# Performance work log

Hardware: AMD Instinct MI355X
Metric: run time of the kernel (lower is better)

## Reference

```python
import jax, jax.numpy as jnp
import numpy as np

N, E, D, ED, L, B = 100000, 1600000, 128, 16, 5, 64
EPS = 1e-5


def _layer_norm(x, w, b):
    mu = jnp.mean(x, axis=-1, keepdims=True)
    var = jnp.mean((x - mu) ** 2, axis=-1, keepdims=True)
    return (x - mu) * jax.lax.rsqrt(var + EPS) * w + b


def setup_inputs() -> dict:
    key = jax.random.key(0)
    ks = jax.random.split(key, 10)
    sc = 0.05
    s = jax.random.normal(ks[0], (N, D), jnp.float32)
    edge_index = jax.random.randint(ks[1], (2, E), 0, N, dtype=jnp.int64)
    edge_attr = jax.random.normal(ks[2], (E, ED), jnp.float32)
    batch = jnp.sort(jax.random.randint(ks[3], (N,), 0, B, dtype=jnp.int64))
    return dict(
        s=s, edge_index=edge_index, edge_attr=edge_attr, batch=batch,
        ln_w=jnp.ones((L, D), jnp.float32),
        ln_b=jnp.zeros((L, D), jnp.float32),
        eW1=jax.random.normal(ks[4], (L, 2 * D + ED, ED), jnp.float32) * sc,
        eb1=jnp.zeros((L, ED), jnp.float32),
        eW2=jax.random.normal(ks[5], (L, ED, ED), jnp.float32) * sc,
        eb2=jnp.zeros((L, ED), jnp.float32),
        nW1=jax.random.normal(ks[6], (L, D + ED, D), jnp.float32) * sc,
        nb1=jnp.zeros((L, D), jnp.float32),
        nW2=jax.random.normal(ks[7], (L, D, D), jnp.float32) * sc,
        nb2=jnp.zeros((L, D), jnp.float32),
    )


def reference(s, edge_index, edge_attr, batch, ln_w, ln_b, eW1, eb1, eW2, eb2, nW1, nb1, nW2, nb2):
    src, dst = edge_index[0], edge_index[1]
    n = s.shape[0]
    num_layers = ln_w.shape[0]
    # scatter-mean denominator (in-degree, clamped to 1)
    deg = jax.ops.segment_sum(jnp.ones((edge_index.shape[1],), s.dtype), dst, num_segments=n)
    deg = jnp.maximum(deg, 1.0)[:, None]
    for i in range(num_layers):
        # per-node LayerNorm over feature dim (vector channel is None)
        s = _layer_norm(s, ln_w[i], ln_b[i])
        # edge message: gather endpoints, concat with edge_attr -> [E, 2D+ED]
        m = jnp.concatenate([s[src], s[dst], edge_attr], axis=-1)
        edge_attr = jax.nn.silu(m @ eW1[i] + eb1[i]) @ eW2[i] + eb2[i]
        # scatter-mean aggregate to destination nodes -> [N, ED]
        agg = jax.ops.segment_sum(edge_attr, dst, num_segments=n) / deg
        h = jnp.concatenate([s, agg], axis=-1)
        out = jax.nn.silu(h @ nW1[i] + nb1[i]) @ nW2[i] + nb2[i]  # discarded, as in original
    return s, edge_attr
```

## Files before the change

kernel.cpp:

```cpp
#include <hip/hip_runtime.h>

#define N_NODES 100000
#define N_EDGES 1600000
#define DIM     128
#define EDIM    16
#define NLAYERS 5

typedef unsigned short ushort_t;
typedef short bf16x8 __attribute__((ext_vector_type(8)));
typedef float f32x4  __attribute__((ext_vector_type(4)));

__device__ __forceinline__ ushort_t f2bf(float f) {
    union { float f; unsigned int i; } c; c.f = f;
    unsigned int r = c.i + 0x7fffu + ((c.i >> 16) & 1u);
    return (ushort_t)(r >> 16);
}
__device__ __forceinline__ float lo_bf(unsigned int w) {
    union { unsigned int i; float f; } c; c.i = w << 16; return c.f;
}
__device__ __forceinline__ float hi_bf(unsigned int w) {
    union { unsigned int i; float f; } c; c.i = w & 0xffff0000u; return c.f;
}
__device__ __forceinline__ unsigned int pk_bf16(float lo, float hi) {
    unsigned int r;
    asm("v_cvt_pk_bf16_f32 %0, %1, %2" : "=v"(r) : "v"(lo), "v"(hi));
    return r;
}
__device__ __forceinline__ bf16x8 pk8(f32x4 a, f32x4 b) {
    union { unsigned int w[4]; bf16x8 v; } c;
    c.w[0] = pk_bf16(a[0], a[1]); c.w[1] = pk_bf16(a[2], a[3]);
    c.w[2] = pk_bf16(b[0], b[1]); c.w[3] = pk_bf16(b[2], b[3]);
    return c.v;
}
__device__ __forceinline__ void lds_fence() {
    asm volatile("s_waitcnt lgkmcnt(0)" ::: "memory");
    __builtin_amdgcn_sched_barrier(0);
}

__global__ void swizzle_weights(const float* __restrict__ eW1,
                                const float* __restrict__ eW2,
                                ushort_t* __restrict__ w1s,
                                ushort_t* __restrict__ w2s) {
    int id = blockIdx.x * 256 + threadIdx.x;
    if (id >= NLAYERS * 10 * 64) return;
    int lane = id & 63;
    int t10 = id >> 6;
    int layer = t10 / 10, t = t10 % 10;
    int n = lane & 15, quad = lane >> 4;
    if (t < 9) {
        ushort_t* dst = w1s + ((size_t)(layer * 9 + t) * 64 + lane) * 8;
        #pragma unroll
        for (int j = 0; j < 8; ++j) {
            int k = t * 32 + quad * 8 + j;
            dst[j] = (k < 2 * DIM + EDIM)
                       ? f2bf(eW1[((size_t)layer * 272 + k) * 16 + n])
                       : (ushort_t)0;
        }
    } else {
        ushort_t* dst = w2s + ((size_t)layer * 64 + lane) * 8;
        #pragma unroll
        for (int j = 0; j < 8; ++j) {
            int k = quad * 8 + j;
            dst[j] = (k < EDIM) ? f2bf(eW2[((size_t)layer * 16 + k) * 16 + n])
                                : (ushort_t)0;
        }
    }
}

__global__ __launch_bounds__(256) void ln_uv(
        const float* __restrict__ sin, float* __restrict__ sout,
        const float* __restrict__ lnw, const float* __restrict__ lnb,
        const ushort_t* __restrict__ w1s,
        ushort_t* __restrict__ u_buf, ushort_t* __restrict__ v_buf,
        int l0, int l1, int lstr) {
    const int wv = threadIdx.x >> 6, lane = threadIdx.x & 63;
    const int m = lane & 15, quad = lane >> 4;
    const int tile = blockIdx.x * 4 + wv;
    if (tile >= N_NODES / 16) return;
    const int node = tile * 16 + m;

    float x[32];
    {
        const float* row = sin + (size_t)node * DIM + quad * 8;
        #pragma unroll
        for (int t = 0; t < 4; ++t) {
            f32x4 a = *(const f32x4*)(row + t * 32);
            f32x4 b = *(const f32x4*)(row + t * 32 + 4);
            #pragma unroll
            for (int j = 0; j < 4; ++j) { x[t * 8 + j] = a[j]; x[t * 8 + 4 + j] = b[j]; }
        }
    }

    for (int li = l0; li < l1; ++li) {
        float s = 0.f;
        #pragma unroll
        for (int k = 0; k < 32; ++k) s += x[k];
        s += __shfl_xor(s, 16); s += __shfl_xor(s, 32);
        float mu = s * (1.0f / DIM);
        float ss = 0.f;
        #pragma unroll
        for (int k = 0; k < 32; ++k) { float d = x[k] - mu; ss += d * d; }
        ss += __shfl_xor(ss, 16); ss += __shfl_xor(ss, 32);
        float rs = rsqrtf(ss * (1.0f / DIM) + 1e-5f);

        const float* w = lnw + (size_t)li * DIM + quad * 8;
        const float* b = lnb + (size_t)li * DIM + quad * 8;
        f32x4 au = {0.f, 0.f, 0.f, 0.f}, av = {0.f, 0.f, 0.f, 0.f};
        #pragma unroll
        for (int t = 0; t < 4; ++t) {
            f32x4 wa = *(const f32x4*)(w + t * 32), wb = *(const f32x4*)(w + t * 32 + 4);
            f32x4 ba = *(const f32x4*)(b + t * 32), bb = *(const f32x4*)(b + t * 32 + 4);
            #pragma unroll
            for (int j = 0; j < 4; ++j) {
                x[t * 8 + j]     = (x[t * 8 + j]     - mu) * rs * wa[j] + ba[j];
                x[t * 8 + 4 + j] = (x[t * 8 + 4 + j] - mu) * rs * wb[j] + bb[j];
            }
            f32x4 ya, yb;
            #pragma unroll
            for (int j = 0; j < 4; ++j) { ya[j] = x[t * 8 + j]; yb[j] = x[t * 8 + 4 + j]; }
            bf16x8 af = pk8(ya, yb);
            bf16x8 bu = *(const bf16x8*)(w1s + ((size_t)(li * 9 + t)     * 64 + lane) * 8);
            bf16x8 bv = *(const bf16x8*)(w1s + ((size_t)(li * 9 + 4 + t) * 64 + lane) * 8);
            au = __builtin_amdgcn_mfma_f32_16x16x32_bf16(bu, af, au, 0, 0, 0);
            av = __builtin_amdgcn_mfma_f32_16x16x32_bf16(bv, af, av, 0, 0, 0);
        }
        size_t rec = ((size_t)node * lstr + (li - l0)) * EDIM + quad * 4;
        uint2 tu; tu.x = pk_bf16(au[0], au[1]); tu.y = pk_bf16(au[2], au[3]);
        uint2 tv; tv.x = pk_bf16(av[0], av[1]); tv.y = pk_bf16(av[2], av[3]);
        *(uint2*)(u_buf + rec) = tu;
        *(uint2*)(v_buf + rec) = tv;
    }

    float* orow = sout + (size_t)node * DIM + quad * 8;
    #pragma unroll
    for (int t = 0; t < 4; ++t) {
        f32x4 a, b;
        #pragma unroll
        for (int j = 0; j < 4; ++j) { a[j] = x[t * 8 + j]; b[j] = x[t * 8 + 4 + j]; }
        *(f32x4*)(orow + t * 32) = a;
        *(f32x4*)(orow + t * 32 + 4) = b;
    }
}

template<int NL>
__global__ __launch_bounds__(256) void edge_fused(
        const float* __restrict__ ea_in, float* __restrict__ ea_out,
        const int* __restrict__ ei,
        const ushort_t* __restrict__ u_buf, const ushort_t* __restrict__ v_buf,
        const ushort_t* __restrict__ w1s, const ushort_t* __restrict__ w2s,
        const float* __restrict__ eb1, const float* __restrict__ eb2,
        int l0) {
    __shared__ ushort_t tbH[4][16 * 24];
    __shared__ ushort_t tbY[4][16 * 24];
    const int wv = threadIdx.x >> 6, lane = threadIdx.x & 63;
    const int m = lane & 15, quad = lane >> 4;

    bf16x8 w1f[NL], w2f[NL];
    f32x4 b1[NL], b2[NL];
    #pragma unroll
    for (int l = 0; l < NL; ++l) {
        w1f[l] = *(const bf16x8*)(w1s + (((size_t)(l0 + l) * 9 + 8) * 64 + lane) * 8);
        w2f[l] = *(const bf16x8*)(w2s + ((size_t)(l0 + l) * 64 + lane) * 8);
        #pragma unroll
        for (int r = 0; r < 4; ++r) {
            b1[l][r] = eb1[(l0 + l) * EDIM + quad * 4 + r];
            b2[l][r] = eb2[(l0 + l) * EDIM + quad * 4 + r];
        }
    }
    ushort_t* tlH = tbH[wv];
    ushort_t* tlY = tbY[wv];
    const bf16x8 zf = {0, 0, 0, 0, 0, 0, 0, 0};
    const int nTiles = N_EDGES / 64;

    for (int tile = blockIdx.x; tile < nTiles; tile += gridDim.x) {
        const int e = tile * 64 + wv * 16 + m;
        const int es = ei[e];
        const int ed = ei[N_EDGES + e];

        uint2 gu[NL], gv[NL];
        #pragma unroll
        for (int l = 0; l < NL; ++l) {
            gu[l] = *(const uint2*)(u_buf + ((size_t)es * NL + l) * EDIM + quad * 4);
            gv[l] = *(const uint2*)(v_buf + ((size_t)ed * NL + l) * EDIM + quad * 4);
        }

        bf16x8 af = zf;
        if (quad < 2) {
            const float* ep = ea_in + (size_t)e * EDIM + quad * 8;
            af = pk8(*(const f32x4*)ep, *(const f32x4*)(ep + 4));
        }

        f32x4 y = {0.f, 0.f, 0.f, 0.f};
        #pragma unroll
        for (int l = 0; l < NL; ++l) {
            f32x4 acc = {0.f, 0.f, 0.f, 0.f};
            acc = __builtin_amdgcn_mfma_f32_16x16x32_bf16(w1f[l], af, acc, 0, 0, 0);
            float x0 = acc[0] + lo_bf(gu[l].x) + lo_bf(gv[l].x) + b1[l][0];
            float x1 = acc[1] + hi_bf(gu[l].x) + hi_bf(gv[l].x) + b1[l][1];
            float x2 = acc[2] + lo_bf(gu[l].y) + lo_bf(gv[l].y) + b1[l][2];
            float x3 = acc[3] + hi_bf(gu[l].y) + hi_bf(gv[l].y) + b1[l][3];
            float h0 = x0 / (1.0f + __expf(-x0));
            float h1 = x1 / (1.0f + __expf(-x1));
            float h2 = x2 / (1.0f + __expf(-x2));
            float h3 = x3 / (1.0f + __expf(-x3));

            uint2 hw; hw.x = pk_bf16(h0, h1); hw.y = pk_bf16(h2, h3);
            *(uint2*)(tlH + m * 24 + quad * 4) = hw;
            lds_fence();
            bf16x8 hf = zf;
            if (quad < 2) hf = *(const bf16x8*)(tlH + m * 24 + quad * 8);

            f32x4 acc2 = {0.f, 0.f, 0.f, 0.f};
            acc2 = __builtin_amdgcn_mfma_f32_16x16x32_bf16(w2f[l], hf, acc2, 0, 0, 0);
            y[0] = acc2[0] + b2[l][0];
            y[1] = acc2[1] + b2[l][1];
            y[2] = acc2[2] + b2[l][2];
            y[3] = acc2[3] + b2[l][3];

            if (l < NL - 1) {
                uint2 yw; yw.x = pk_bf16(y[0], y[1]); yw.y = pk_bf16(y[2], y[3]);
                *(uint2*)(tlY + m * 24 + quad * 4) = yw;
                lds_fence();
                af = zf;
                if (quad < 2) af = *(const bf16x8*)(tlY + m * 24 + quad * 8);
            }
        }
        *(f32x4*)(ea_out + (size_t)e * EDIM + quad * 4) = y;
    }
}

extern "C" void kernel_launch(void* const* d_in, const int* in_sizes, int n_in,
                              void* d_out, int out_size, void* d_ws, size_t ws_size,
                              hipStream_t stream) {
    const float* s_in  = (const float*)d_in[0];
    const int*   ei    = (const int*)d_in[1];
    const float* ea_in = (const float*)d_in[2];
    const float* lnw = (const float*)d_in[4];
    const float* lnb = (const float*)d_in[5];
    const float* eW1 = (const float*)d_in[6];
    const float* eb1 = (const float*)d_in[7];
    const float* eW2 = (const float*)d_in[8];
    const float* eb2 = (const float*)d_in[9];

    float* out_s  = (float*)d_out;
    float* out_ea = (float*)d_out + (size_t)N_NODES * DIM;

    ushort_t* w1s = (ushort_t*)d_ws;
    ushort_t* w2s = w1s + (size_t)NLAYERS * 9 * 64 * 8;
    ushort_t* uv0 = w2s + (size_t)NLAYERS * 64 * 8;
    const size_t wWords  = (size_t)NLAYERS * 10 * 64 * 8;
    const size_t uvLayer = (size_t)N_NODES * EDIM;
    const size_t needFused = (wWords + 2 * (size_t)NLAYERS * uvLayer) * 2;
    const int lnGrid = (N_NODES / 16 + 3) / 4;
    const int eGrid = 4096;

    swizzle_weights<<<13, 256, 0, stream>>>(eW1, eW2, w1s, w2s);

    if (ws_size >= needFused) {
        ushort_t* u0 = uv0;
        ushort_t* v0 = u0 + (size_t)NLAYERS * uvLayer;
        ln_uv<<<lnGrid, 256, 0, stream>>>(s_in, out_s, lnw, lnb, w1s,
                                          u0, v0, 0, NLAYERS, NLAYERS);
        edge_fused<NLAYERS><<<eGrid, 256, 0, stream>>>(ea_in, out_ea, ei, u0, v0,
                                                       w1s, w2s, eb1, eb2, 0);
    } else {
        ushort_t* u0 = uv0;
        ushort_t* v0 = u0 + uvLayer;
        for (int l = 0; l < NLAYERS; ++l) {
            ln_uv<<<lnGrid, 256, 0, stream>>>(l == 0 ? s_in : out_s, out_s,
                                              lnw, lnb, w1s, u0, v0, l, l + 1, 1);
            edge_fused<1><<<eGrid, 256, 0, stream>>>(
                l == 0 ? ea_in : (const float*)out_ea, out_ea, ei, u0, v0,
                w1s, w2s, eb1, eb2, l);
        }
    }
}
```

Measured before the change: 442.4 us.

## Software-pipeline edge gathers across tiles and use fast reciprocal SiLU

Restructures the per-tile edge loop so that the u/v gathers and edge-attribute loads for the next tile, and the edge indices for the tile after that, are issued before computing the current tile. This hides the latency of the dependent index-then-gather chain behind the MFMA and SiLU work. SiLU also switches from a true divide to a hardware reciprocal approximation. The cost is more live registers for the doubled gather buffers, which may reduce occupancy, plus slightly less precise SiLU.

```diff
diff --git a/kernel.cpp b/kernel.cpp
--- a/kernel.cpp
+++ b/kernel.cpp
@@ -31,6 +31,9 @@
     c.w[0] = pk_bf16(a[0], a[1]); c.w[1] = pk_bf16(a[2], a[3]);
     c.w[2] = pk_bf16(b[0], b[1]); c.w[3] = pk_bf16(b[2], b[3]);
     return c.v;
+}
+__device__ __forceinline__ float fast_silu(float x) {
+    return x * __builtin_amdgcn_rcpf(1.0f + __expf(-x));
 }
 __device__ __forceinline__ void lds_fence() {
     asm volatile("s_waitcnt lgkmcnt(0)" ::: "memory");
@@ -170,39 +173,78 @@
     ushort_t* tlH = tbH[wv];
     ushort_t* tlY = tbY[wv];
     const bf16x8 zf = {0, 0, 0, 0, 0, 0, 0, 0};
+    const f32x4 z4 = {0.f, 0.f, 0.f, 0.f};
     const int nTiles = N_EDGES / 64;
-
-    for (int tile = blockIdx.x; tile < nTiles; tile += gridDim.x) {
-        const int e = tile * 64 + wv * 16 + m;
-        const int es = ei[e];
-        const int ed = ei[N_EDGES + e];
-
-        uint2 gu[NL], gv[NL];
+    const int stride = gridDim.x;
+
+    int tile = blockIdx.x;
+    if (tile >= nTiles) return;
+
+    uint2 gu[NL], gv[NL];
+    f32x4 ea_a = z4, ea_b = z4;
+    int es_n, ed_n;
+    {
+        const int e0 = tile * 64 + wv * 16 + m;
+        const int es = ei[e0];
+        const int ed = ei[N_EDGES + e0];
         #pragma unroll
         for (int l = 0; l < NL; ++l) {
             gu[l] = *(const uint2*)(u_buf + ((size_t)es * NL + l) * EDIM + quad * 4);
             gv[l] = *(const uint2*)(v_buf + ((size_t)ed * NL + l) * EDIM + quad * 4);
         }
+        if (quad < 2) {
+            const float* ep = ea_in + (size_t)e0 * EDIM + quad * 8;
+            ea_a = *(const f32x4*)ep; ea_b = *(const f32x4*)(ep + 4);
+        }
+        const int t1 = tile + stride;
+        const int e1 = (t1 < nTiles ? t1 : tile) * 64 + wv * 16 + m;
+        es_n = ei[e1];
+        ed_n = ei[N_EDGES + e1];
+    }
+
+    for (; tile < nTiles; tile += stride) {
+        const int tn = tile + stride;
+        const bool hn = tn < nTiles;
+        const int tc = hn ? tn : tile;
+
+        uint2 gun[NL], gvn[NL];
+        #pragma unroll
+        for (int l = 0; l < NL; ++l) {
+            gun[l] = *(const uint2*)(u_buf + ((size_t)es_n * NL + l) * EDIM + quad * 4);
+            gvn[l] = *(const uint2*)(v_buf + ((size_t)ed_n * NL + l) * EDIM + quad * 4);
+        }
+        f32x4 ean_a = z4, ean_b = z4;
+        {
+            const int en = tc * 64 + wv * 16 + m;
+            if (quad < 2) {
+                const float* ep = ea_in + (size_t)en * EDIM + quad * 8;
+                ean_a = *(const f32x4*)ep; ean_b = *(const f32x4*)(ep + 4);
+            }
+        }
+        int es_nn, ed_nn;
+        {
+            const int t2 = tn + stride;
+            const int e2 = (t2 < nTiles ? t2 : tc) * 64 + wv * 16 + m;
+            es_nn = ei[e2];
+            ed_nn = ei[N_EDGES + e2];
+        }
 
         bf16x8 af = zf;
-        if (quad < 2) {
-            const float* ep = ea_in + (size_t)e * EDIM + quad * 8;
-            af = pk8(*(const f32x4*)ep, *(const f32x4*)(ep + 4));
-        }
-
-        f32x4 y = {0.f, 0.f, 0.f, 0.f};
+        if (quad < 2) af = pk8(ea_a, ea_b);
+
+        f32x4 y = z4;
         #pragma unroll
         for (int l = 0; l < NL; ++l) {
-            f32x4 acc = {0.f, 0.f, 0.f, 0.f};
+            f32x4 acc = z4;
             acc = __builtin_amdgcn_mfma_f32_16x16x32_bf16(w1f[l], af, acc, 0, 0, 0);
             float x0 = acc[0] + lo_bf(gu[l].x) + lo_bf(gv[l].x) + b1[l][0];
             float x1 = acc[1] + hi_bf(gu[l].x) + hi_bf(gv[l].x) + b1[l][1];
             float x2 = acc[2] + lo_bf(gu[l].y) + lo_bf(gv[l].y) + b1[l][2];
             float x3 = acc[3] + hi_bf(gu[l].y) + hi_bf(gv[l].y) + b1[l][3];
-            float h0 = x0 / (1.0f + __expf(-x0));
-            float h1 = x1 / (1.0f + __expf(-x1));
-            float h2 = x2 / (1.0f + __expf(-x2));
-            float h3 = x3 / (1.0f + __expf(-x3));
+            float h0 = fast_silu(x0);
+            float h1 = fast_silu(x1);
+            float h2 = fast_silu(x2);
+            float h3 = fast_silu(x3);
 
             uint2 hw; hw.x = pk_bf16(h0, h1); hw.y = pk_bf16(h2, h3);
             *(uint2*)(tlH + m * 24 + quad * 4) = hw;
@@ -210,7 +252,7 @@
             bf16x8 hf = zf;
             if (quad < 2) hf = *(const bf16x8*)(tlH + m * 24 + quad * 8);
 
-            f32x4 acc2 = {0.f, 0.f, 0.f, 0.f};
+            f32x4 acc2 = z4;
             acc2 = __builtin_amdgcn_mfma_f32_16x16x32_bf16(w2f[l], hf, acc2, 0, 0, 0);
             y[0] = acc2[0] + b2[l][0];
             y[1] = acc2[1] + b2[l][1];
@@ -225,7 +267,13 @@
                 if (quad < 2) af = *(const bf16x8*)(tlY + m * 24 + quad * 8);
             }
         }
+        const int e = tile * 64 + wv * 16 + m;
         *(f32x4*)(ea_out + (size_t)e * EDIM + quad * 4) = y;
+
+        #pragma unroll
+        for (int l = 0; l < NL; ++l) { gu[l] = gun[l]; gv[l] = gvn[l]; }
+        ea_a = ean_a; ea_b = ean_b;
+        es_n = es_nn; ed_n = ed_nn;
     }
 }
 
```

After: 434.9 us. No clear change (-1.7%).
